# Kernel optimization log

Measured on AMD Instinct MI355X. Metric: run time of the kernel, lower is better.

Reference implementation:

```python
import jax, jax.numpy as jnp
from jax import lax
import numpy as np

DG = 2          # deformable groups
KH = KW = 3     # kernel size
KK = KH * KW
PAD = 1


def setup_inputs() -> dict:
    key = jax.random.key(0)
    k1, k2, k3 = jax.random.split(key, 3)
    B, C, H, W = 4, 64, 128, 128
    O = 64
    x = jax.random.normal(k1, (B, C, H, W), jnp.float32)
    # original inits offset weights to 0 (degenerate: plain conv); use small random
    # weights instead so the irregular bilinear-gather path is actually exercised.
    w_off = jax.random.normal(k2, (DG * 2 * KK, C, KH, KW), jnp.float32) * 0.05
    w_def = jax.random.normal(k3, (O, C, KH, KW), jnp.float32) * (1.0 / np.sqrt(C * KK))
    return {"x": x, "w_off": w_off, "w_def": w_def}


def _deform_conv(x, w_off, w_def):
    B, C, H, W = x.shape
    O = w_def.shape[0]
    Cg = C // DG

    # offset = offset_conv(x): stride 1, pad 1, no bias -> [B, DG*2*KK, H, W]
    offset = lax.conv_general_dilated(
        x, w_off, window_strides=(1, 1), padding=((PAD, PAD), (PAD, PAD)),
        dimension_numbers=("NCHW", "OIHW", "NCHW"))
    # DCN layout: per group, per kernel tap k, channel 2k = dy, 2k+1 = dx
    off = offset.reshape(B, DG, KK, 2, H, W)

    ki, kj = jnp.meshgrid(jnp.arange(KH), jnp.arange(KW), indexing="ij")
    ki = (ki.reshape(KK) - PAD).astype(x.dtype)   # kernel row offsets -1..1
    kj = (kj.reshape(KK) - PAD).astype(x.dtype)
    hh = jnp.arange(H, dtype=x.dtype)
    ww = jnp.arange(W, dtype=x.dtype)

    # sampling positions [B, DG, KK, H, W]
    py = off[:, :, :, 0] + ki[None, None, :, None, None] + hh[None, None, None, :, None]
    px = off[:, :, :, 1] + kj[None, None, :, None, None] + ww[None, None, None, None, :]

    y0 = jnp.floor(py).astype(jnp.int32)
    x0 = jnp.floor(px).astype(jnp.int32)
    dy = py - y0.astype(x.dtype)
    dx = px - x0.astype(x.dtype)

    x_g = x.reshape(B, DG, Cg, H * W)

    def gather(yi, xi):
        # zero padding outside the image
        valid = ((yi >= 0) & (yi < H) & (xi >= 0) & (xi < W)).astype(x.dtype)
        yc = jnp.clip(yi, 0, H - 1)
        xc = jnp.clip(xi, 0, W - 1)
        idx = (yc * W + xc).reshape(B, DG, 1, KK * H * W)
        v = jnp.take_along_axis(x_g, idx, axis=3).reshape(B, DG, Cg, KK, H, W)
        return v * valid[:, :, None]  # broadcast over channel axis

    # bilinear interpolation at learned offset positions
    val = (gather(y0, x0) * ((1 - dy) * (1 - dx))[:, :, None]
           + gather(y0, x0 + 1) * ((1 - dy) * dx)[:, :, None]
           + gather(y0 + 1, x0) * (dy * (1 - dx))[:, :, None]
           + gather(y0 + 1, x0 + 1) * (dy * dx)[:, :, None])

    # weighted accumulation: conv groups = 1, channel dim = DG*Cg
    w = w_def.reshape(O, DG, Cg, KK)
    return jnp.einsum("bgckhw,ogck->bohw", val, w)


def reference(x, w_off, w_def):
    return _deform_conv(x, w_off, w_def)
```

## Files before the change

kernel.cpp:

```cpp
#include <hip/hip_runtime.h>
#include <hip/hip_bf16.h>

typedef _Float16 f16x8 __attribute__((ext_vector_type(8)));
typedef _Float16 f16x2 __attribute__((ext_vector_type(2)));
typedef float f32x4  __attribute__((ext_vector_type(4)));

#define Bn 4
#define Cn 64
#define Hn 128
#define Wn 128
#define HWn 16384

#define XT_BYTES    (Bn*HWn*Cn*2)
#define PKDEF_BYTES (18*4*64*8*2)

static __device__ __forceinline__ unsigned pk_f16(float lo, float hi) {
  union { _Float16 h[2]; unsigned u; } cv;
  cv.h[0] = (_Float16)lo; cv.h[1] = (_Float16)hi;
  return cv.u;
}

__global__ __launch_bounds__(256) void prep_all(const float* __restrict__ x,
                                                const float* __restrict__ w_off,
                                                const float* __restrict__ w_def,
                                                ushort* __restrict__ xt,
                                                ushort* __restrict__ pk_def,
                                                ushort* __restrict__ pk_off) {
  __shared__ float tile[64][68];
  const int t = threadIdx.x;
  const int blk = blockIdx.x;
  if (blk < 1024) {
    const int b = blk >> 8;
    const int pix0 = (blk & 255) * 64;
    const int y = pix0 >> 7, x0 = pix0 & 127;
    const float* xb = x + (b * Cn) * HWn + pix0;
#pragma unroll
    for (int q = 0; q < 4; ++q) {
      int idx = q * 256 + t;
      int c = idx >> 4, p4 = idx & 15;
      float4 v = *(const float4*)(xb + c * HWn + p4 * 4);
      *(float4*)&tile[c][p4 * 4] = v;
    }
    __syncthreads();
    const int p = t & 63, cg = t >> 6;
#pragma unroll
    for (int half = 0; half < 2; ++half) {
      const int seg = cg * 2 + half;
      unsigned u[4];
#pragma unroll
      for (int j = 0; j < 4; ++j)
        u[j] = pk_f16(tile[seg * 8 + 2 * j][p], tile[seg * 8 + 2 * j + 1][p]);
      uint4 v = {u[0], u[1], u[2], u[3]};
      *(uint4*)(xt + (((((b << 7) + y) << 3) + seg) * 128 + x0 + p) * 8) = v;
    }
  } else {
    const int tt = (blk - 1024) * 256 + t;
    if (tt < 4608) {
      int lane = tt & 63, oc = (tt >> 6) & 3, s = tt >> 8;
      int g = s / 9, k = s % 9;
      int o = oc * 16 + (lane & 15);
      int cb = g * 32 + (lane >> 4) * 8;
      unsigned u[4];
#pragma unroll
      for (int j = 0; j < 4; ++j)
        u[j] = pk_f16(w_def[(o * Cn + cb + 2 * j) * 9 + k],
                      w_def[(o * Cn + cb + 2 * j + 1) * 9 + k]);
      uint4 v = {u[0], u[1], u[2], u[3]};
      *(uint4*)(pk_def + tt * 8) = v;
    } else if (tt < 8064) {
      int t2 = tt - 4608;
      int lane = t2 & 63, r = t2 >> 6;
      int oc = r % 3, s = r / 3;
      int k = s >> 1, chalf = s & 1;
      int o = oc * 16 + (lane & 15);
      int cb = chalf * 32 + (lane >> 4) * 8;
      unsigned u[4];
#pragma unroll
      for (int j = 0; j < 4; ++j) {
        float lo = (o < 36) ? w_off[(o * Cn + cb + 2 * j) * 9 + k] : 0.f;
        float hi = (o < 36) ? w_off[(o * Cn + cb + 2 * j + 1) * 9 + k] : 0.f;
        u[j] = pk_f16(lo, hi);
      }
      uint4 v = {u[0], u[1], u[2], u[3]};
      *(uint4*)(pk_off + (r * 64 + lane) * 8) = v;
    }
  }
}

#define T_STRIDE (17*25*8)
__global__ __launch_bounds__(1024, 8) void deform_fused(const ushort* __restrict__ xt,
                                                        const ushort* __restrict__ pk_def,
                                                        const ushort* __restrict__ pk_off,
                                                        float* __restrict__ out) {
  __shared__ ushort tile[8 * T_STRIDE];
  __shared__ _Float16 off_lds[8][36][18];
  const int t = threadIdx.x;
  const int lane = t & 63;
  const int wid = t >> 6;
  const int pg = wid >> 1, gsel = wid & 1;
  int bid = blockIdx.x;
  bid = (bid & 7) * 64 + (bid >> 3);
  const int b  = bid >> 7;
  const int ty = (bid >> 3) & 15;
  const int tx = bid & 7;
  const int y0t = ty * 8, x0t = tx * 16;
  const int TLY = max(0, y0t - 4), THY = min(127, y0t + 12);
  const int TLX = max(0, x0t - 4), THX = min(127, x0t + 20);
  const int Hd = THY - TLY + 1, Wd = THX - TLX + 1;

  {
    const int xq = t & 31;
    const int r0 = t >> 5;
    const int nr = Hd * 8;
    for (int rr = r0; rr < nr; rr += 32) {
      const int yq = rr >> 3, seg = rr & 7;
      if (xq < Wd) {
        const ushort* src = xt + ((((b << 7) + TLY + yq) << 3) + seg) * 1024 + (TLX + xq) * 8;
        *(uint4*)&tile[seg * T_STRIDE + (yq * 25 + xq) * 8] = *(const uint4*)src;
      }
    }
  }
  __syncthreads();

  const int h = y0t + pg;
  const int p = lane & 15, kq = lane >> 4;
  const int w_ = x0t + p;
  const int pixin = (h << 7) + x0t;
  const int su = gsel * 4 + kq;
  const int colb = lane & 15;

  int pixoff[9]; bool tvalid[9];
#pragma unroll
  for (int kk = 0; kk < 9; ++kk) {
    int yk = h + kk / 3 - 1, xk = w_ + kk % 3 - 1;
    tvalid[kk] = ((unsigned)yk < 128u) && ((unsigned)xk < 128u);
    int yc = min(max(yk, 0), 127), xc = min(max(xk, 0), 127);
    pixoff[kk] = ((yc - TLY) * 25 + (xc - TLX)) * 8;
  }

  {
    f32x4 oa0 = {0,0,0,0}, oa1 = {0,0,0,0}, oa2 = {0,0,0,0};
    const f16x8* pBo = (const f16x8*)pk_off;
#pragma unroll
    for (int s = 0; s < 18; ++s) {
      const int k = s >> 1, chalf = s & 1;
      uint4 t_ = *(const uint4*)&tile[(chalf * 4 + kq) * T_STRIDE + pixoff[k]];
      if (!tvalid[k]) { t_.x = 0; t_.y = 0; t_.z = 0; t_.w = 0; }
      union { uint4 u; f16x8 v; } A; A.u = t_;
      if (gsel == 0) {
        oa0 = __builtin_amdgcn_mfma_f32_16x16x32_f16(A.v, pBo[(s*3 + 0)*64 + lane], oa0, 0,0,0);
      } else {
        oa1 = __builtin_amdgcn_mfma_f32_16x16x32_f16(A.v, pBo[(s*3 + 1)*64 + lane], oa1, 0,0,0);
        oa2 = __builtin_amdgcn_mfma_f32_16x16x32_f16(A.v, pBo[(s*3 + 2)*64 + lane], oa2, 0,0,0);
      }
    }
    if (gsel == 0) {
#pragma unroll
      for (int r = 0; r < 4; ++r) off_lds[pg][colb][kq * 4 + r] = (_Float16)oa0[r];
    } else {
#pragma unroll
      for (int r = 0; r < 4; ++r) {
        off_lds[pg][16 + colb][kq * 4 + r] = (_Float16)oa1[r];
        if (colb < 4) off_lds[pg][32 + colb][kq * 4 + r] = (_Float16)oa2[r];
      }
    }
  }
  __syncthreads();

  float offv[18];
#pragma unroll
  for (int j = 0; j < 18; ++j) offv[j] = (float)off_lds[pg][gsel * 18 + j][p];

  f32x4 acc0={0,0,0,0}, acc1={0,0,0,0}, acc2={0,0,0,0}, acc3={0,0,0,0};
  const f16x8* pB = (const f16x8*)pk_def;

#pragma unroll
  for (int j = 0; j < 9; ++j) {
    const int k = j;
    float py = offv[2*j]   + (float)(h  + k / 3 - 1);
    float px = offv[2*j+1] + (float)(w_ + k % 3 - 1);
    float fy = floorf(py), fx = floorf(px);
    int y0 = (int)fy, x0 = (int)fx;
    float dy = py - fy, dx = px - fx;

    bool vy0 = (y0 >= 0) && (y0 < Hn);
    bool vy1 = (y0 >= -1) && (y0 < Hn - 1);
    bool vx0 = (x0 >= 0) && (x0 < Wn);
    bool vx1 = (x0 >= -1) && (x0 < Wn - 1);
    float omdy = 1.f - dy, omdx = 1.f - dx;
    float w00 = (vy0 && vx0) ? omdy * omdx : 0.f;
    float w01 = (vy0 && vx1) ? omdy * dx   : 0.f;
    float w10 = (vy1 && vx0) ? dy * omdx   : 0.f;
    float w11 = (vy1 && vx1) ? dy * dx     : 0.f;

    int iy0 = min(max(y0, 0), Hn - 1), iy1 = min(max(y0 + 1, 0), Hn - 1);
    int ix0 = min(max(x0, 0), Wn - 1), ix1 = min(max(x0 + 1, 0), Wn - 1);

    uint4 c00, c01, c10, c11;
    bool intile = (iy0 >= TLY) && (iy1 <= THY) && (ix0 >= TLX) && (ix1 <= THX);
    if (__all((int)intile)) {
      const int base = su * T_STRIDE;
      const int ly0 = iy0 - TLY, ly1 = iy1 - TLY;
      const int lx0 = ix0 - TLX, lx1 = ix1 - TLX;
      c00 = *(const uint4*)&tile[base + (ly0 * 25 + lx0) * 8];
      c01 = *(const uint4*)&tile[base + (ly0 * 25 + lx1) * 8];
      c10 = *(const uint4*)&tile[base + (ly1 * 25 + lx0) * 8];
      c11 = *(const uint4*)&tile[base + (ly1 * 25 + lx1) * 8];
    } else {
      const int r0g = ((((b << 7) + iy0) << 3) + su) * 128;
      const int r1g = ((((b << 7) + iy1) << 3) + su) * 128;
      c00 = *(const uint4*)(xt + (r0g + ix0) * 8);
      c01 = *(const uint4*)(xt + (r0g + ix1) * 8);
      c10 = *(const uint4*)(xt + (r1g + ix0) * 8);
      c11 = *(const uint4*)(xt + (r1g + ix1) * 8);
    }

    const _Float16 h00 = (_Float16)w00, h01 = (_Float16)w01;
    const _Float16 h10 = (_Float16)w10, h11 = (_Float16)w11;
    const f16x2 W00 = {h00, h00}, W01 = {h01, h01};
    const f16x2 W10 = {h10, h10}, W11 = {h11, h11};
    union U32H { unsigned u; f16x2 h; };
    union { uint4 u; f16x8 v; } A;
#define BILC(comp, fld)                                                        \
    { U32H a0, a1, a2, a3, r;                                                  \
      a0.u = c00.comp; a1.u = c01.comp; a2.u = c10.comp; a3.u = c11.comp;      \
      r.h = a0.h * W00 + a1.h * W01 + a2.h * W10 + a3.h * W11;                 \
      A.u.fld = r.u; }
    BILC(x, x) BILC(y, y) BILC(z, z) BILC(w, w)
#undef BILC

    const int s = gsel * 9 + j;
    acc0 = __builtin_amdgcn_mfma_f32_16x16x32_f16(A.v, pB[(s*4 + 0)*64 + lane], acc0, 0,0,0);
    acc1 = __builtin_amdgcn_mfma_f32_16x16x32_f16(A.v, pB[(s*4 + 1)*64 + lane], acc1, 0,0,0);
    acc2 = __builtin_amdgcn_mfma_f32_16x16x32_f16(A.v, pB[(s*4 + 2)*64 + lane], acc2, 0,0,0);
    acc3 = __builtin_amdgcn_mfma_f32_16x16x32_f16(A.v, pB[(s*4 + 3)*64 + lane], acc3, 0,0,0);
  }

  __syncthreads();
  float* red = (float*)tile;
  if (gsel == 1) {
    *(f32x4*)&red[((pg * 4 + 0) * 64 + lane) * 4] = acc0;
    *(f32x4*)&red[((pg * 4 + 1) * 64 + lane) * 4] = acc1;
    *(f32x4*)&red[((pg * 4 + 2) * 64 + lane) * 4] = acc2;
    *(f32x4*)&red[((pg * 4 + 3) * 64 + lane) * 4] = acc3;
  }
  __syncthreads();
  if (gsel == 0) {
    acc0 += *(const f32x4*)&red[((pg * 4 + 0) * 64 + lane) * 4];
    acc1 += *(const f32x4*)&red[((pg * 4 + 1) * 64 + lane) * 4];
    acc2 += *(const f32x4*)&red[((pg * 4 + 2) * 64 + lane) * 4];
    acc3 += *(const f32x4*)&red[((pg * 4 + 3) * 64 + lane) * 4];
    float* ob = out + pixin + kq * 4;
#pragma unroll
    for (int r = 0; r < 4; ++r) {
      ob[((b*64 +      colb) << 14) + r] = acc0[r];
      ob[((b*64 + 16 + colb) << 14) + r] = acc1[r];
      ob[((b*64 + 32 + colb) << 14) + r] = acc2[r];
      ob[((b*64 + 48 + colb) << 14) + r] = acc3[r];
    }
  }
}

extern "C" void kernel_launch(void* const* d_in, const int* in_sizes, int n_in,
                              void* d_out, int out_size, void* d_ws, size_t ws_size,
                              hipStream_t stream) {
  const float* x     = (const float*)d_in[0];
  const float* w_off = (const float*)d_in[1];
  const float* w_def = (const float*)d_in[2];
  float* out = (float*)d_out;

  char* ws = (char*)d_ws;
  ushort* xt     = (ushort*)ws;
  ushort* pk_def = (ushort*)(ws + XT_BYTES);
  ushort* pk_off = (ushort*)(ws + XT_BYTES + PKDEF_BYTES);

  prep_all<<<1056, 256, 0, stream>>>(x, w_off, w_def, xt, pk_def, pk_off);
  deform_fused<<<512, 1024, 0, stream>>>(xt, pk_def, pk_off, out);
}
```

Measured before the change: 47.18 us.

## Load only conv-needed rows before sync, defer halo rows behind offset MFMA

The initial tile load now fetches only the rows the offset convolution needs (tile rows y0t-1..y0t+8). The remaining halo rows are loaded into registers after the first barrier and written to LDS after the offset MFMA phase. This overlaps the halo global-memory latency with offset computation and shortens the critical path before the first barrier. In exchange it adds register pressure (two uint4 per thread) at a launch bound of 1024 threads, and it loads clamped duplicate columns at the right edge.

```diff
diff --git a/kernel.cpp b/kernel.cpp
--- a/kernel.cpp
+++ b/kernel.cpp
@@ -106,21 +106,45 @@
   const int y0t = ty * 8, x0t = tx * 16;
   const int TLY = max(0, y0t - 4), THY = min(127, y0t + 12);
   const int TLX = max(0, x0t - 4), THX = min(127, x0t + 20);
-  const int Hd = THY - TLY + 1, Wd = THX - TLX + 1;
+  const int Wd = THX - TLX + 1;
+  const int CLO = max(0, y0t - 1), CHI = min(127, y0t + 8);
 
   {
     const int xq = t & 31;
     const int r0 = t >> 5;
-    const int nr = Hd * 8;
-    for (int rr = r0; rr < nr; rr += 32) {
+    const int nrc = (CHI - CLO + 1) * 8;
+    for (int rr = r0; rr < nrc; rr += 32) {
       const int yq = rr >> 3, seg = rr & 7;
+      const int gy = CLO + yq;
       if (xq < Wd) {
-        const ushort* src = xt + ((((b << 7) + TLY + yq) << 3) + seg) * 1024 + (TLX + xq) * 8;
-        *(uint4*)&tile[seg * T_STRIDE + (yq * 25 + xq) * 8] = *(const uint4*)src;
+        const ushort* src = xt + ((((b << 7) + gy) << 3) + seg) * 1024 + (TLX + xq) * 8;
+        *(uint4*)&tile[seg * T_STRIDE + ((gy - TLY) * 25 + xq) * 8] = *(const uint4*)src;
       }
     }
   }
   __syncthreads();
+
+  const int nlow = CLO - TLY, nhigh = THY - CHI;
+  const int nhalo = (nlow + nhigh) * 8 * 25;
+  uint4 hu0, hu1; int hl0 = -1, hl1 = -1;
+  {
+    int fi = t;
+    if (fi < nhalo) {
+      int xq = fi % 25; int r = fi / 25; int seg = r & 7; int hr = r >> 3;
+      int gy = (hr < nlow) ? (TLY + hr) : (CHI + 1 + hr - nlow);
+      int gx = min(TLX + xq, 127);
+      hu0 = *(const uint4*)(xt + ((((b << 7) + gy) << 3) + seg) * 1024 + gx * 8);
+      hl0 = seg * T_STRIDE + ((gy - TLY) * 25 + xq) * 8;
+    }
+    fi = t + 1024;
+    if (fi < nhalo) {
+      int xq = fi % 25; int r = fi / 25; int seg = r & 7; int hr = r >> 3;
+      int gy = (hr < nlow) ? (TLY + hr) : (CHI + 1 + hr - nlow);
+      int gx = min(TLX + xq, 127);
+      hu1 = *(const uint4*)(xt + ((((b << 7) + gy) << 3) + seg) * 1024 + gx * 8);
+      hl1 = seg * T_STRIDE + ((gy - TLY) * 25 + xq) * 8;
+    }
+  }
 
   const int h = y0t + pg;
   const int p = lane & 15, kq = lane >> 4;
@@ -165,6 +189,9 @@
       }
     }
   }
+
+  if (hl0 >= 0) *(uint4*)&tile[hl0] = hu0;
+  if (hl1 >= 0) *(uint4*)&tile[hl1] = hu1;
   __syncthreads();
 
   float offv[18];
```

Measured after the change: 47.02 us (median of 2 runs). Within noise of the previous version (-0.4%).
